# Kernel optimization log

Hardware: AMD Instinct MI355X
Metric: run time of the kernel (lower is better)

The kernel has to match this reference:

```python
import jax, jax.numpy as jnp
import numpy as np

B, S, D, H, R, P = 4, 8192, 512, 8, 64, 4
HD = D // H  # 64
EPS = 1e-6


def _sketch_p4(z, G1, G2):
    # sketchwithnegativity(z, 2): M1 = M2 = z
    inv_sqrt_r = 1.0 / np.sqrt(R).astype(np.float32)
    half = inv_sqrt_r * ((z @ G1) * (z @ G2))  # [B,H,S,R]
    return half * half  # sketch(): half * half for p=4


def setup_inputs() -> dict:
    key = jax.random.key(0)
    ks = jax.random.split(key, 16)
    lin = lambda k: jax.random.normal(k, (D, D), jnp.float32) * (1.0 / np.sqrt(D))
    g = lambda k: jax.random.normal(k, (HD, R), jnp.float32) * (1.0 / np.sqrt(R))
    return {
        "x": jax.random.normal(ks[0], (B, S, D), jnp.float32),
        "Wq": lin(ks[1]), "bq": jnp.zeros((D,), jnp.float32),
        "Wk": lin(ks[2]), "bk": jnp.zeros((D,), jnp.float32),
        "Wv": lin(ks[3]), "bv": jnp.zeros((D,), jnp.float32),
        "Wp": lin(ks[4]), "bp": jnp.zeros((D,), jnp.float32),
        "gamma_q": jnp.ones((1,), jnp.float32), "beta_q": jnp.zeros((1,), jnp.float32),
        "gamma_k": jnp.ones((1,), jnp.float32), "beta_k": jnp.zeros((1,), jnp.float32),
        "qG1": g(ks[5]), "qG2": g(ks[6]),
        "kG1": g(ks[7]), "kG2": g(ks[8]),
    }


def reference(x, Wq, bq, Wk, bk, Wv, bv, Wp, bp,
              gamma_q, beta_q, gamma_k, beta_k, qG1, qG2, kG1, kG2):
    b, s, d = x.shape
    split = lambda t: t.reshape(b, s, H, HD).transpose(0, 2, 1, 3)  # [B,H,S,HD]
    q = split(x @ Wq + bq)
    k = split(x @ Wk + bk)
    v = split(x @ Wv + bv)
    q = gamma_q * q + beta_q
    k = gamma_k * k + beta_k
    phi_q = _sketch_p4(q, qG1, qG2)  # [B,H,S,R]
    phi_k = _sketch_p4(k, kG1, kG2)  # [B,H,S,R]
    # linear-attention form of attn = (phi_q phi_k^T) / rowsum; avoids [S,S]
    kv = jnp.einsum('bhsr,bhsd->bhrd', phi_k, v)          # [B,H,R,HD]
    ksum = phi_k.sum(axis=2)                              # [B,H,R]
    num = jnp.einsum('bhqr,bhrd->bhqd', phi_q, kv)        # [B,H,S,HD]
    den = jnp.einsum('bhqr,bhr->bhq', phi_q, ksum) + EPS  # [B,H,S]
    out = num / den[..., None]
    out = out.transpose(0, 2, 1, 3).reshape(b, s, d)
    return out @ Wp + bp
```

## Files before the change

kernel.cpp:

```cpp
#include <hip/hip_runtime.h>
#include <hip/hip_bf16.h>


#define SEQ 8192

typedef __attribute__((ext_vector_type(8))) short bf16x8;
typedef __attribute__((ext_vector_type(4))) float f32x4;

__device__ __forceinline__ unsigned short f2b(float f) {
    union { float f; unsigned int i; } v; v.f = f;
    unsigned int r = v.i + 0x7fffu + ((v.i >> 16) & 1u);
    return (unsigned short)(r >> 16);
}
__device__ __forceinline__ float b2f(unsigned short u) {
    union { unsigned int i; float f; } v; v.i = ((unsigned int)u) << 16; return v.f;
}

#if __has_builtin(__builtin_amdgcn_global_load_lds)
#define ASYNC_CP 1
#endif

__device__ __forceinline__ void cp16(const unsigned short* g, unsigned short* l) {
#ifdef ASYNC_CP
    __builtin_amdgcn_global_load_lds(
        (const __attribute__((address_space(1))) unsigned int*)g,
        (__attribute__((address_space(3))) unsigned int*)l, 16, 0, 0);
#endif
}

__global__ __launch_bounds__(256) void prep_all(
    const float* __restrict__ x, unsigned short* __restrict__ xb,
    const float* __restrict__ Wv, const float* __restrict__ Wp,
    unsigned short* __restrict__ WTf, unsigned short* __restrict__ WTp,
    const float* __restrict__ Wq, const float* __restrict__ bq,
    const float* __restrict__ Wk, const float* __restrict__ bk,
    const float* __restrict__ bv,
    const float* __restrict__ gq, const float* __restrict__ bbq,
    const float* __restrict__ gk, const float* __restrict__ bbk,
    const float* __restrict__ qG1, const float* __restrict__ qG2,
    const float* __restrict__ kG1, const float* __restrict__ kG2,
    float* __restrict__ cvec)
{
    const int blk = blockIdx.x;
    const int tid = threadIdx.x;

    if (blk < 8192) {
        size_t i = ((size_t)blk * 256 + tid) * 8;
        float4 a = *(const float4*)&x[i];
        float4 b = *(const float4*)&x[i + 4];
        ushort4 o1 = { f2b(a.x), f2b(a.y), f2b(a.z), f2b(a.w) };
        ushort4 o2 = { f2b(b.x), f2b(b.y), f2b(b.z), f2b(b.w) };
        *(ushort4*)&xb[i]     = o1;
        *(ushort4*)&xb[i + 4] = o2;
        return;
    }

    if (blk < 8704) {
        const int idx = blk - 8192;
        const int z = idx >> 8;
        const float* W = (z == 0) ? Wv : Wp;
        unsigned short* O = (z == 0) ? (WTf + (size_t)2048 * 512) : WTp;
        __shared__ float t[32][33];
        const int tx = tid & 31, ty = tid >> 5;
        const int k0 = ((idx >> 4) & 15) * 32, n0 = (idx & 15) * 32;
        #pragma unroll
        for (int i = 0; i < 4; ++i)
            t[ty + 8 * i][tx] = W[(size_t)(k0 + ty + 8 * i) * 512 + n0 + tx];
        __syncthreads();
        #pragma unroll
        for (int i = 0; i < 4; ++i)
            O[(size_t)(n0 + ty + 8 * i) * 512 + k0 + tx] = f2b(t[tx][ty + 8 * i]);
        return;
    }

    const int idx = blk - 8704;
    if (idx == 512) {
        for (int i = tid; i < 512; i += 256) cvec[2048 + i] = bv[i];
        return;
    }
    const int bi = idx & 31, ky = idx >> 5;
    const int zz = bi >> 4, h = (bi >> 1) & 7, p = bi & 1;
    const float* W    = zz ? Wk : Wq;
    const float* bias = zz ? bk : bq;
    const float* G    = zz ? (p ? kG2 : kG1) : (p ? qG2 : qG1);
    const float  gamma = zz ? gk[0] : gq[0];
    const float  beta  = zz ? bbk[0] : bbq[0];

    __shared__ float Gs[64][65];
    for (int i = tid; i < 4096; i += 256) Gs[i >> 6][i & 63] = G[i];
    __syncthreads();

    const int rr = tid & 63, kg = tid >> 6;
    const int jc = zz * 1024 + h * 128 + rr * 2 + p;
    const int k0 = ky * 32;
    for (int k = k0 + kg; k < k0 + 32; k += 4) {
        float s = 0.f;
        const float* wrow = &W[(size_t)k * 512 + h * 64];
        #pragma unroll 8
        for (int j = 0; j < 64; ++j) s = fmaf(wrow[j], Gs[j][rr], s);
        WTf[(size_t)jc * 512 + k] = f2b(gamma * s);
    }
    if (kg == 0 && ky == 0) {
        float cb = 0.f, cg = 0.f;
        #pragma unroll 8
        for (int j = 0; j < 64; ++j) {
            cb = fmaf(bias[h * 64 + j], Gs[j][rr], cb);
            cg += Gs[j][rr];
        }
        cvec[jc] = gamma * cb + beta * cg;
    }
}

__global__ __launch_bounds__(256) void gemm_mfma_fused(
    const unsigned short* __restrict__ xb,
    const unsigned short* __restrict__ WTf,
    const float* __restrict__ cvec,
    unsigned short* __restrict__ PHIQ, unsigned short* __restrict__ PHIKT,
    unsigned short* __restrict__ VT)
{
    __shared__ __align__(16) unsigned short smem[9216];
    unsigned short* As = smem;
    unsigned short* Bs = smem + 4096;
    unsigned short* ep = smem;

    const int tid = threadIdx.x;
    const int w = tid >> 6, lane = tid & 63;
    const int j0 = blockIdx.x * 128;
    const int n0 = blockIdx.y * 128;
    const int wr = w >> 1, wc = w & 1;

    const int r0 = w * 32 + (lane >> 2);
    const int kq = (lane & 3) * 8;
    const unsigned short* gA = &xb[(size_t)(n0 + r0) * 512 + kq];
    const unsigned short* gB = &WTf[(size_t)(j0 + r0) * 512 + kq];
    unsigned short* lA = As + (w * 32) * 32;
    unsigned short* lB = Bs + (w * 32) * 32;

    f32x4 acc[4][4];
    #pragma unroll
    for (int i = 0; i < 4; ++i)
        #pragma unroll
        for (int j = 0; j < 4; ++j) { acc[i][j] = (f32x4){0.f, 0.f, 0.f, 0.f}; }

    const int cr = (lane >> 4) * 8;

    for (int k0 = 0; k0 < 512; k0 += 32) {
        __syncthreads();
#ifdef ASYNC_CP
        cp16(gA + k0, lA);
        cp16(gA + 16 * 512 + k0, lA + 16 * 32);
        cp16(gB + k0, lB);
        cp16(gB + 16 * 512 + k0, lB + 16 * 32);
#else
        { uint4 v = *(const uint4*)(gA + k0);            *(uint4*)(lA + (size_t)lane * 8) = v; }
        { uint4 v = *(const uint4*)(gA + 16 * 512 + k0); *(uint4*)(lA + 16 * 32 + (size_t)lane * 8) = v; }
        { uint4 v = *(const uint4*)(gB + k0);            *(uint4*)(lB + (size_t)lane * 8) = v; }
        { uint4 v = *(const uint4*)(gB + 16 * 512 + k0); *(uint4*)(lB + 16 * 32 + (size_t)lane * 8) = v; }
#endif
        __syncthreads();

        bf16x8 af[4], bfr[4];
        #pragma unroll
        for (int i = 0; i < 4; ++i) {
            af[i]  = *(const bf16x8*)&As[(wr * 64 + i * 16 + (lane & 15)) * 32 + cr];
            bfr[i] = *(const bf16x8*)&Bs[(wc * 64 + i * 16 + (lane & 15)) * 32 + cr];
        }
        #pragma unroll
        for (int mi = 0; mi < 4; ++mi)
            #pragma unroll
            for (int ni = 0; ni < 4; ++ni)
                acc[mi][ni] = __builtin_amdgcn_mfma_f32_16x16x32_bf16(
                    af[mi], bfr[ni], acc[mi][ni], 0, 0, 0);
    }

    __syncthreads();
    const int bq = n0 >> 13;
    const int sq = n0 & (SEQ - 1);

    if (j0 < 1024) {
        const int h = j0 >> 7;
        #pragma unroll
        for (int ni = 0; ni < 4; ++ni) {
            const int loc = wc * 64 + ni * 16 + (lane & 15);
            const float cv = cvec[j0 + loc];
            const int rr = loc >> 1;
            #pragma unroll
            for (int mi = 0; mi < 4; ++mi)
                #pragma unroll
                for (int r = 0; r < 4; ++r) {
                    float u = acc[mi][ni][r] + cv;
                    float up = __shfl_xor(u, 1);
                    float hh = 0.125f * u * up;
                    float phi = hh * hh;
                    if ((lane & 1) == 0)
                        ep[(wr * 64 + mi * 16 + (lane >> 4) * 4 + r) * 72 + rr] = f2b(phi);
                }
        }
        __syncthreads();
        for (int i = tid; i < 1024; i += 256) {
            const int tok = i >> 3, ch = i & 7;
            *(uint4*)&PHIQ[((size_t)(bq * 8 + h) * SEQ + sq + tok) * 64 + ch * 8] =
                *(const uint4*)&ep[tok * 72 + ch * 8];
        }
    } else if (j0 < 2048) {
        const int h = (j0 >> 7) & 7;
        #pragma unroll
        for (int ni = 0; ni < 4; ++ni) {
            const int loc = wc * 64 + ni * 16 + (lane & 15);
            const float cv = cvec[j0 + loc];
            const int rr = loc >> 1;
            #pragma unroll
            for (int mi = 0; mi < 4; ++mi)
                #pragma unroll
                for (int r = 0; r < 4; ++r) {
                    float u = acc[mi][ni][r] + cv;
                    float up = __shfl_xor(u, 1);
                    float hh = 0.125f * u * up;
                    float phi = hh * hh;
                    if ((lane & 1) == 0)
                        ep[rr * 136 + wr * 64 + mi * 16 + (lane >> 4) * 4 + r] = f2b(phi);
                }
        }
        __syncthreads();
        for (int i = tid; i < 1024; i += 256) {
            const int row = i >> 4, ch = i & 15;
            *(uint4*)&PHIKT[((size_t)((bq * 8 + h) * 64 + row)) * SEQ + sq + ch * 8] =
                *(const uint4*)&ep[row * 136 + ch * 8];
        }
    } else {
        #pragma unroll
        for (int half = 0; half < 2; ++half) {
            if (wc == half) {
                #pragma unroll
                for (int ni = 0; ni < 4; ++ni) {
                    const int loc = ni * 16 + (lane & 15);
                    const float cv = cvec[j0 + half * 64 + loc];
                    #pragma unroll
                    for (int mi = 0; mi < 4; ++mi)
                        #pragma unroll
                        for (int r = 0; r < 4; ++r)
                            ep[loc * 136 + wr * 64 + mi * 16 + (lane >> 4) * 4 + r] =
                                f2b(acc[mi][ni][r] + cv);
                }
            }
            __syncthreads();
            for (int i = tid; i < 1024; i += 256) {
                const int row = i >> 4, ch = i & 15;
                const int n = (j0 - 2048) + half * 64 + row;
                *(uint4*)&VT[((size_t)(bq * 512 + n)) * SEQ + sq + ch * 8] =
                    *(const uint4*)&ep[row * 136 + ch * 8];
            }
            __syncthreads();
        }
    }
}

__global__ __launch_bounds__(256) void gemm_mfma_final(
    const unsigned short* __restrict__ Ab,
    const unsigned short* __restrict__ WTp,
    const float* __restrict__ bias, float* __restrict__ out)
{
    __shared__ __align__(16) unsigned short As[128 * 32];
    __shared__ __align__(16) unsigned short Bs[128 * 32];

    const int tid = threadIdx.x;
    const int w = tid >> 6, lane = tid & 63;
    const int j0 = blockIdx.x * 128;
    const int n0 = blockIdx.y * 128;
    const int wr = w >> 1, wc = w & 1;

    const int r0 = w * 32 + (lane >> 2);
    const int kq = (lane & 3) * 8;
    const unsigned short* gA = &Ab[(size_t)(n0 + r0) * 512 + kq];
    const unsigned short* gB = &WTp[(size_t)(j0 + r0) * 512 + kq];
    unsigned short* lA = &As[(w * 32) * 32];
    unsigned short* lB = &Bs[(w * 32) * 32];

    f32x4 acc[4][4];
    #pragma unroll
    for (int i = 0; i < 4; ++i)
        #pragma unroll
        for (int j = 0; j < 4; ++j) { acc[i][j] = (f32x4){0.f, 0.f, 0.f, 0.f}; }

    const int cr = (lane >> 4) * 8;

    for (int k0 = 0; k0 < 512; k0 += 32) {
        __syncthreads();
#ifdef ASYNC_CP
        cp16(gA + k0, lA);
        cp16(gA + 16 * 512 + k0, lA + 16 * 32);
        cp16(gB + k0, lB);
        cp16(gB + 16 * 512 + k0, lB + 16 * 32);
#else
        { uint4 v = *(const uint4*)(gA + k0);            *(uint4*)(lA + (size_t)lane * 8) = v; }
        { uint4 v = *(const uint4*)(gA + 16 * 512 + k0); *(uint4*)(lA + 16 * 32 + (size_t)lane * 8) = v; }
        { uint4 v = *(const uint4*)(gB + k0);            *(uint4*)(lB + (size_t)lane * 8) = v; }
        { uint4 v = *(const uint4*)(gB + 16 * 512 + k0); *(uint4*)(lB + 16 * 32 + (size_t)lane * 8) = v; }
#endif
        __syncthreads();

        bf16x8 af[4], bfr[4];
        #pragma unroll
        for (int i = 0; i < 4; ++i) {
            af[i]  = *(const bf16x8*)&As[(wr * 64 + i * 16 + (lane & 15)) * 32 + cr];
            bfr[i] = *(const bf16x8*)&Bs[(wc * 64 + i * 16 + (lane & 15)) * 32 + cr];
        }
        #pragma unroll
        for (int mi = 0; mi < 4; ++mi)
            #pragma unroll
            for (int ni = 0; ni < 4; ++ni)
                acc[mi][ni] = __builtin_amdgcn_mfma_f32_16x16x32_bf16(
                    af[mi], bfr[ni], acc[mi][ni], 0, 0, 0);
    }

    #pragma unroll
    for (int ni = 0; ni < 4; ++ni) {
        const int jcol = j0 + wc * 64 + ni * 16 + (lane & 15);
        const float bvv = bias[jcol];
        #pragma unroll
        for (int mi = 0; mi < 4; ++mi) {
            #pragma unroll
            for (int r = 0; r < 4; ++r) {
                const int t = n0 + wr * 64 + mi * 16 + (lane >> 4) * 4 + r;
                out[(size_t)t * 512 + jcol] = acc[mi][ni][r] + bvv;
            }
        }
    }
}

__global__ __launch_bounds__(256) void kv_mfma(
    const unsigned short* __restrict__ PHIKT, const unsigned short* __restrict__ VT,
    float* __restrict__ KVP, float* __restrict__ KSP)
{
    const int bh = blockIdx.x, seg = blockIdx.y;
    const int tid = threadIdx.x;
    const int w = tid >> 6, lane = tid & 63;
    const size_t pbase =
        ((size_t)bh * 64 + w * 16 + (lane & 15)) * SEQ + seg * 512 + (lane >> 4) * 8;
    const size_t vbase =
        ((size_t)((bh >> 3) * 512 + (bh & 7) * 64 + (lane & 15))) * SEQ
        + seg * 512 + (lane >> 4) * 8;

    f32x4 acc[4], ks;
    #pragma unroll
    for (int nt = 0; nt < 4; ++nt) acc[nt] = (f32x4){0.f, 0.f, 0.f, 0.f};
    ks = (f32x4){0.f, 0.f, 0.f, 0.f};
    bf16x8 ones;
    #pragma unroll
    for (int i = 0; i < 8; ++i) ones[i] = (short)0x3f80;

    #pragma unroll 2
    for (int k = 0; k < 512; k += 32) {
        bf16x8 a = *(const bf16x8*)&PHIKT[pbase + k];
        ks = __builtin_amdgcn_mfma_f32_16x16x32_bf16(a, ones, ks, 0, 0, 0);
        #pragma unroll
        for (int nt = 0; nt < 4; ++nt) {
            bf16x8 bb = *(const bf16x8*)&VT[vbase + (size_t)nt * 16 * SEQ + k];
            acc[nt] = __builtin_amdgcn_mfma_f32_16x16x32_bf16(a, bb, acc[nt], 0, 0, 0);
        }
    }

    float* kvp = &KVP[((size_t)bh * 16 + seg) * 4096];
    #pragma unroll
    for (int nt = 0; nt < 4; ++nt) {
        float4 o = { acc[nt][0], acc[nt][1], acc[nt][2], acc[nt][3] };
        *(float4*)&kvp[(nt * 16 + (lane & 15)) * 64 + w * 16 + (lane >> 4) * 4] = o;
    }
    if ((lane & 15) == 0) {
        float4 o = { ks[0], ks[1], ks[2], ks[3] };
        *(float4*)&KSP[((size_t)bh * 16 + seg) * 64 + w * 16 + (lane >> 4) * 4] = o;
    }
}

__global__ __launch_bounds__(256) void kv_reduce(
    const float* __restrict__ KVP, const float* __restrict__ KSP,
    float* __restrict__ KV, float* __restrict__ KS)
{
    const int bh = blockIdx.x;
    const int e0 = blockIdx.y * 512;
    for (int e = e0 + threadIdx.x; e < e0 + 512; e += 256) {
        float s = 0.f;
        #pragma unroll 8
        for (int c = 0; c < 16; ++c) s += KVP[(size_t)(bh * 16 + c) * 4096 + e];
        KV[(size_t)bh * 4096 + e] = s;
    }
    if (blockIdx.y == 0 && threadIdx.x < 64) {
        float s = 0.f;
        for (int c = 0; c < 16; ++c) s += KSP[(bh * 16 + c) * 64 + threadIdx.x];
        KS[bh * 64 + threadIdx.x] = s;
    }
}

__global__ __launch_bounds__(256) void attn_mfma(
    const unsigned short* __restrict__ PHIQ, const float* __restrict__ KV,
    const float* __restrict__ KS, unsigned short* __restrict__ OAb)
{
    __shared__ __align__(16) unsigned short bpad[144 * 72];
    const int bh = blockIdx.x, st = blockIdx.y;
    const int tid = threadIdx.x;
    const int b = bh >> 3, h = bh & 7;

    for (int i = tid; i < 144 * 64; i += 256) {
        const int n = i >> 6, r = i & 63;
        float val;
        if (n < 64)        val = KV[(size_t)bh * 4096 + n * 64 + r];
        else if (n < 128)  { float x = KV[(size_t)bh * 4096 + (n - 64) * 64 + r];
                             val = x - b2f(f2b(x)); }
        else if (n == 128) val = KS[bh * 64 + r];
        else if (n == 129) { float x = KS[bh * 64 + r]; val = x - b2f(f2b(x)); }
        else               val = 0.f;
        bpad[n * 72 + r] = f2b(val);
    }
    __syncthreads();

    const int w = tid >> 6, lane = tid & 63;
    bf16x8 bf[9][2];
    #pragma unroll
    for (int nt = 0; nt < 9; ++nt) {
        const unsigned short* bp = &bpad[(nt * 16 + (lane & 15)) * 72 + (lane >> 4) * 8];
        bf[nt][0] = *(const bf16x8*)bp;
        bf[nt][1] = *(const bf16x8*)(bp + 32);
    }

    const int tw = st * 256 + w * 64;
    #pragma unroll
    for (int mt = 0; mt < 4; ++mt) {
        const unsigned short* ap =
            &PHIQ[((size_t)bh * SEQ + tw + mt * 16 + (lane & 15)) * 64 + (lane >> 4) * 8];
        bf16x8 a0 = *(const bf16x8*)ap;
        bf16x8 a1 = *(const bf16x8*)(ap + 32);
        f32x4 acc[9];
        #pragma unroll
        for (int nt = 0; nt < 9; ++nt) acc[nt] = (f32x4){0.f, 0.f, 0.f, 0.f};
        #pragma unroll
        for (int nt = 0; nt < 9; ++nt) {
            acc[nt] = __builtin_amdgcn_mfma_f32_16x16x32_bf16(a0, bf[nt][0], acc[nt], 0, 0, 0);
            acc[nt] = __builtin_amdgcn_mfma_f32_16x16x32_bf16(a1, bf[nt][1], acc[nt], 0, 0, 0);
        }
        #pragma unroll
        for (int r4 = 0; r4 < 4; ++r4) {
            const float den = __shfl(acc[8][r4], (lane & 48)) +
                              __shfl(acc[8][r4], (lane & 48) + 1) + 1e-6f;
            const float inv = 1.0f / den;
            const int s = tw + mt * 16 + (lane >> 4) * 4 + r4;
            #pragma unroll
            for (int nt = 0; nt < 4; ++nt)
                OAb[((size_t)b * SEQ + s) * 512 + h * 64 + nt * 16 + (lane & 15)] =
                    f2b((acc[nt][r4] + acc[nt + 4][r4]) * inv);
        }
    }
}

extern "C" void kernel_launch(void* const* d_in, const int* in_sizes, int n_in,
                              void* d_out, int out_size, void* d_ws, size_t ws_size,
                              hipStream_t stream)
{
    (void)in_sizes; (void)n_in; (void)out_size; (void)ws_size;
    const float* x   = (const float*)d_in[0];
    const float* Wq  = (const float*)d_in[1];
    const float* bq  = (const float*)d_in[2];
    const float* Wk  = (const float*)d_in[3];
    const float* bk  = (const float*)d_in[4];
    const float* Wv  = (const float*)d_in[5];
    const float* bv  = (const float*)d_in[6];
    const float* Wp  = (const float*)d_in[7];
    const float* bp  = (const float*)d_in[8];
    const float* gq  = (const float*)d_in[9];
    const float* bbq = (const float*)d_in[10];
    const float* gk  = (const float*)d_in[11];
    const float* bbk = (const float*)d_in[12];
    const float* qG1 = (const float*)d_in[13];
    const float* qG2 = (const float*)d_in[14];
    const float* kG1 = (const float*)d_in[15];
    const float* kG2 = (const float*)d_in[16];

    unsigned short* PHIQ  = (unsigned short*)d_ws;
    unsigned short* PHIKT = PHIQ + 16777216;
    unsigned short* VT    = PHIKT + 16777216;
    unsigned short* xb    = VT   + 16777216;
    unsigned short* OAb   = xb   + 16777216;
    unsigned short* WTf   = OAb  + 16777216;
    unsigned short* WTp   = WTf  + 2560 * 512;
    float* cvec = (float*)(WTp + 262144);
    float* KVP  = cvec + 2560;
    float* KSP  = KVP + 4194304;
    float* KV   = KSP + 65536;
    float* KS   = KV + 131072;
    float* out  = (float*)d_out;

    hipLaunchKernelGGL(prep_all, dim3(9217), dim3(256), 0, stream,
                       x, xb, Wv, Wp, WTf, WTp,
                       Wq, bq, Wk, bk, bv, gq, bbq, gk, bbk,
                       qG1, qG2, kG1, kG2, cvec);
    hipLaunchKernelGGL(gemm_mfma_fused, dim3(20, 256), dim3(256), 0, stream,
                       xb, WTf, cvec, PHIQ, PHIKT, VT);
    hipLaunchKernelGGL(kv_mfma, dim3(32, 16), dim3(256), 0, stream,
                       PHIKT, VT, KVP, KSP);
    hipLaunchKernelGGL(kv_reduce, dim3(32, 8), dim3(256), 0, stream, KVP, KSP, KV, KS);
    hipLaunchKernelGGL(attn_mfma, dim3(32, 32), dim3(256), 0, stream,
                       PHIQ, KV, KS, OAb);
    hipLaunchKernelGGL(gemm_mfma_final, dim3(4, 256), dim3(256), 0, stream,
                       OAb, WTp, bp, out);
}
```

Before: 432.3 us.

## Remap GEMM blocks per XCD and store epilogue directly without LDS staging

Both GEMM kernels switch to a 1-D grid whose block index is remapped so that consecutive blocks on the same XCD share row tiles of the activation matrix. The aim is better L2 reuse of the A operand across the 8 XCDs. The fused QKV GEMM epilogue also drops the LDS transpose and its barriers and writes PHIQ, PHIKT and VT straight from registers. Those direct stores are narrow and scattered (2-byte PHIQ stores, 8-byte ushort4 for the transposed outputs), which may hurt write coalescing compared with the earlier 16-byte staged stores.

```diff
diff --git a/kernel.cpp b/kernel.cpp
--- a/kernel.cpp
+++ b/kernel.cpp
@@ -118,23 +118,23 @@
     unsigned short* __restrict__ PHIQ, unsigned short* __restrict__ PHIKT,
     unsigned short* __restrict__ VT)
 {
-    __shared__ __align__(16) unsigned short smem[9216];
-    unsigned short* As = smem;
-    unsigned short* Bs = smem + 4096;
-    unsigned short* ep = smem;
+    __shared__ __align__(16) unsigned short As[128 * 32];
+    __shared__ __align__(16) unsigned short Bs[128 * 32];
 
     const int tid = threadIdx.x;
     const int w = tid >> 6, lane = tid & 63;
-    const int j0 = blockIdx.x * 128;
-    const int n0 = blockIdx.y * 128;
+    const int flat = blockIdx.x;
+    const int xcd = flat & 7, slot = flat >> 3;
+    const int n0 = (xcd * 32 + slot / 20) * 128;
+    const int j0 = (slot % 20) * 128;
     const int wr = w >> 1, wc = w & 1;
 
     const int r0 = w * 32 + (lane >> 2);
     const int kq = (lane & 3) * 8;
     const unsigned short* gA = &xb[(size_t)(n0 + r0) * 512 + kq];
     const unsigned short* gB = &WTf[(size_t)(j0 + r0) * 512 + kq];
-    unsigned short* lA = As + (w * 32) * 32;
-    unsigned short* lB = Bs + (w * 32) * 32;
+    unsigned short* lA = &As[(w * 32) * 32];
+    unsigned short* lB = &Bs[(w * 32) * 32];
 
     f32x4 acc[4][4];
     #pragma unroll
@@ -173,84 +173,54 @@
                     af[mi], bfr[ni], acc[mi][ni], 0, 0, 0);
     }
 
-    __syncthreads();
     const int bq = n0 >> 13;
     const int sq = n0 & (SEQ - 1);
-
-    if (j0 < 1024) {
-        const int h = j0 >> 7;
+    const int t0 = sq + wr * 64 + (lane >> 4) * 4;
+
+    if (j0 < 2048) {
+        const int zq = j0 >> 10;
+        const int h  = (j0 >> 7) & 7;
         #pragma unroll
         for (int ni = 0; ni < 4; ++ni) {
             const int loc = wc * 64 + ni * 16 + (lane & 15);
             const float cv = cvec[j0 + loc];
             const int rr = loc >> 1;
             #pragma unroll
-            for (int mi = 0; mi < 4; ++mi)
+            for (int mi = 0; mi < 4; ++mi) {
+                float ph[4];
                 #pragma unroll
                 for (int r = 0; r < 4; ++r) {
                     float u = acc[mi][ni][r] + cv;
                     float up = __shfl_xor(u, 1);
                     float hh = 0.125f * u * up;
-                    float phi = hh * hh;
-                    if ((lane & 1) == 0)
-                        ep[(wr * 64 + mi * 16 + (lane >> 4) * 4 + r) * 72 + rr] = f2b(phi);
+                    ph[r] = hh * hh;
                 }
-        }
-        __syncthreads();
-        for (int i = tid; i < 1024; i += 256) {
-            const int tok = i >> 3, ch = i & 7;
-            *(uint4*)&PHIQ[((size_t)(bq * 8 + h) * SEQ + sq + tok) * 64 + ch * 8] =
-                *(const uint4*)&ep[tok * 72 + ch * 8];
-        }
-    } else if (j0 < 2048) {
-        const int h = (j0 >> 7) & 7;
+                if ((lane & 1) == 0) {
+                    if (zq == 0) {
+                        #pragma unroll
+                        for (int r = 0; r < 4; ++r)
+                            PHIQ[((size_t)(bq * 8 + h) * SEQ + t0 + mi * 16 + r) * 64 + rr]
+                                = f2b(ph[r]);
+                    } else {
+                        ushort4 o = { f2b(ph[0]), f2b(ph[1]), f2b(ph[2]), f2b(ph[3]) };
+                        *(ushort4*)&PHIKT[((size_t)((bq * 8 + h) * 64 + rr)) * SEQ
+                                          + t0 + mi * 16] = o;
+                    }
+                }
+            }
+        }
+    } else {
         #pragma unroll
         for (int ni = 0; ni < 4; ++ni) {
             const int loc = wc * 64 + ni * 16 + (lane & 15);
+            const int n = (j0 - 2048) + loc;
             const float cv = cvec[j0 + loc];
-            const int rr = loc >> 1;
-            #pragma unroll
-            for (int mi = 0; mi < 4; ++mi)
-                #pragma unroll
-                for (int r = 0; r < 4; ++r) {
-                    float u = acc[mi][ni][r] + cv;
-                    float up = __shfl_xor(u, 1);
-                    float hh = 0.125f * u * up;
-                    float phi = hh * hh;
-                    if ((lane & 1) == 0)
-                        ep[rr * 136 + wr * 64 + mi * 16 + (lane >> 4) * 4 + r] = f2b(phi);
-                }
-        }
-        __syncthreads();
-        for (int i = tid; i < 1024; i += 256) {
-            const int row = i >> 4, ch = i & 15;
-            *(uint4*)&PHIKT[((size_t)((bq * 8 + h) * 64 + row)) * SEQ + sq + ch * 8] =
-                *(const uint4*)&ep[row * 136 + ch * 8];
-        }
-    } else {
-        #pragma unroll
-        for (int half = 0; half < 2; ++half) {
-            if (wc == half) {
-                #pragma unroll
-                for (int ni = 0; ni < 4; ++ni) {
-                    const int loc = ni * 16 + (lane & 15);
-                    const float cv = cvec[j0 + half * 64 + loc];
-                    #pragma unroll
-                    for (int mi = 0; mi < 4; ++mi)
-                        #pragma unroll
-                        for (int r = 0; r < 4; ++r)
-                            ep[loc * 136 + wr * 64 + mi * 16 + (lane >> 4) * 4 + r] =
-                                f2b(acc[mi][ni][r] + cv);
-                }
+            #pragma unroll
+            for (int mi = 0; mi < 4; ++mi) {
+                ushort4 o = { f2b(acc[mi][ni][0] + cv), f2b(acc[mi][ni][1] + cv),
+                              f2b(acc[mi][ni][2] + cv), f2b(acc[mi][ni][3] + cv) };
+                *(ushort4*)&VT[((size_t)(bq * 512 + n)) * SEQ + t0 + mi * 16] = o;
             }
-            __syncthreads();
-            for (int i = tid; i < 1024; i += 256) {
-                const int row = i >> 4, ch = i & 15;
-                const int n = (j0 - 2048) + half * 64 + row;
-                *(uint4*)&VT[((size_t)(bq * 512 + n)) * SEQ + sq + ch * 8] =
-                    *(const uint4*)&ep[row * 136 + ch * 8];
-            }
-            __syncthreads();
         }
     }
 }
@@ -265,8 +235,10 @@
 
     const int tid = threadIdx.x;
     const int w = tid >> 6, lane = tid & 63;
-    const int j0 = blockIdx.x * 128;
-    const int n0 = blockIdx.y * 128;
+    const int flat = blockIdx.x;
+    const int xcd = flat & 7, slot = flat >> 3;
+    const int n0 = (xcd * 32 + (slot >> 2)) * 128;
+    const int j0 = (slot & 3) * 128;
     const int wr = w >> 1, wc = w & 1;
 
     const int r0 = w * 32 + (lane >> 2);
@@ -492,13 +464,13 @@
                        x, xb, Wv, Wp, WTf, WTp,
                        Wq, bq, Wk, bk, bv, gq, bbq, gk, bbk,
                        qG1, qG2, kG1, kG2, cvec);
-    hipLaunchKernelGGL(gemm_mfma_fused, dim3(20, 256), dim3(256), 0, stream,
+    hipLaunchKernelGGL(gemm_mfma_fused, dim3(5120), dim3(256), 0, stream,
                        xb, WTf, cvec, PHIQ, PHIKT, VT);
     hipLaunchKernelGGL(kv_mfma, dim3(32, 16), dim3(256), 0, stream,
                        PHIKT, VT, KVP, KSP);
     hipLaunchKernelGGL(kv_reduce, dim3(32, 8), dim3(256), 0, stream, KVP, KSP, KV, KS);
     hipLaunchKernelGGL(attn_mfma, dim3(32, 32), dim3(256), 0, stream,
                        PHIQ, KV, KS, OAb);
-    hipLaunchKernelGGL(gemm_mfma_final, dim3(4, 256), dim3(256), 0, stream,
+    hipLaunchKernelGGL(gemm_mfma_final, dim3(1024), dim3(256), 0, stream,
                        OAb, WTp, bp, out);
 }
```

After: 409.0 us. 5.4% less time.
